# Optimization experiments

Hardware: AMD Instinct MI355X
Metric: run time of the kernel (lower is better)

The kernel has to match this reference:

```python
import jax, jax.numpy as jnp
import numpy as np

N = 8192      # nodes; also input feature dim (x.shape[0] used as in_channels)
E = 524288    # edges per edge type (avg degree 64)
H = 200       # hidden dim (hard-coded in RecomNet)
MEAN_RATING = 3.5


def setup_inputs() -> dict:
    key = jax.random.key(0)
    ks = jax.random.split(key, 14)
    s_in = np.float32(1.0 / np.sqrt(N))
    s_h = np.float32(1.0 / np.sqrt(H))
    return {
        "x": jax.random.normal(ks[0], (N, N), jnp.float32),
        "edge_sim": jax.random.randint(ks[1], (2, E), 0, N),
        "edge_rat": jax.random.randint(ks[2], (2, E), 0, N),
        "mask": jax.random.randint(ks[3], (E,), 0, 2).astype(bool),
        # conv1 params (in=N, out=H)
        "w1_self": jax.random.normal(ks[4], (N, H), jnp.float32) * s_in,
        "w1_sim": jax.random.normal(ks[5], (N, H), jnp.float32) * s_in,
        "w1_rat": jax.random.normal(ks[6], (N, H), jnp.float32) * s_in,
        "b1": jnp.zeros((H,), jnp.float32),
        # conv2 params (in=H, out=H)
        "w2_self": jax.random.normal(ks[7], (H, H), jnp.float32) * s_h,
        "w2_sim": jax.random.normal(ks[8], (H, H), jnp.float32) * s_h,
        "w2_rat": jax.random.normal(ks[9], (H, H), jnp.float32) * s_h,
        "b2": jnp.zeros((H,), jnp.float32),
        # bilinear decoder
        "Q": jax.random.normal(ks[10], (H, H), jnp.float32) * s_h,
    }


def _recom_conv(edge_sim, edge_rat, x, w_self, w_sim, w_rat, b):
    # linear-then-gather-then-scatter (linear commutes with sum aggregation)
    m_sim = (x @ w_sim)[edge_sim[0]]                                   # [E, H]
    agg_sim = jax.ops.segment_sum(m_sim, edge_sim[1], num_segments=N)  # [N, H]
    m_rat = (x @ w_rat)[edge_rat[0]]
    agg_rat = jax.ops.segment_sum(m_rat, edge_rat[1], num_segments=N)
    return x @ w_self + agg_sim + agg_rat + b


def reference(x, w1_self, w1_sim, w1_rat, b1, w2_self, w2_sim, w2_rat, b2, Q,
              edge_sim, edge_rat, mask):
    h = _recom_conv(edge_sim, edge_rat, x, w1_self, w1_sim, w1_rat, b1)
    h = jax.nn.relu(h)
    h = _recom_conv(edge_sim, edge_rat, h, w2_self, w2_sim, w2_rat, b2)
    h1 = h[edge_rat[0]]                                                # [E, H]
    h2 = h[edge_rat[1]]                                                # [E, H]
    pred = jnp.einsum("eh,hk,ek->e", h1, Q, h2) + MEAN_RATING          # [E]
    # original compacts with boolean mask (dynamic shape); here we keep a
    # fixed [E] output and zero out unmasked edges
    return jnp.where(mask, pred, 0.0)
```

## Files before the change

kernel.cpp:

```cpp
#include <hip/hip_runtime.h>

#define NN 8192
#define EE 524288
#define HPAD 256
#define NP 640

using s16x8 = __attribute__((ext_vector_type(8))) short;
using f32x4 = __attribute__((ext_vector_type(4))) float;

__device__ __forceinline__ unsigned short f2b(float f) {
    unsigned u = __float_as_uint(f);
    u = (u + 0x7FFFu + ((u >> 16) & 1u)) >> 16;
    return (unsigned short)u;
}
__device__ __forceinline__ float b2f(unsigned short u) {
    return __uint_as_float((unsigned)u << 16);
}

__device__ __forceinline__ void async16(const unsigned short* g, unsigned short* l)
{
    __builtin_amdgcn_global_load_lds(
        (const __attribute__((address_space(1))) unsigned int*)g,
        (__attribute__((address_space(3))) unsigned int*)l, 16, 0, 0);
}


__global__ void cvt_f2b_kernel(const float* __restrict__ in,
                               unsigned short* __restrict__ out, int n4)
{
    int i = blockIdx.x * 256 + threadIdx.x;
    if (i >= n4) return;
    float4 v = ((const float4*)in)[i];
    ushort4 o;
    o.x = f2b(v.x); o.y = f2b(v.y); o.z = f2b(v.z); o.w = f2b(v.w);
    ((ushort4*)out)[i] = o;
}

__global__ void transpose_w_kernel(const float* __restrict__ w0,
                                   const float* __restrict__ w1,
                                   const float* __restrict__ w2,
                                   unsigned short* __restrict__ out,
                                   int Kout, int Kreal, int Nreal)
{
    __shared__ float tile[32][33];
    const int kb = blockIdx.x << 5;
    const int nb = blockIdx.y << 5;
    const int tx = threadIdx.x, ty = threadIdx.y;
    const int n = nb + tx;
    const float* w = (n < 200) ? w0 : (n < 400) ? w1 : w2;
    const int c = (n < 200) ? n : (n < 400) ? n - 200 : n - 400;
#pragma unroll
    for (int i = 0; i < 4; ++i) {
        const int k = kb + ty + (i << 3);
        float v = 0.f;
        if (n < Nreal && k < Kreal) v = w[(size_t)k * 200 + c];
        tile[ty + (i << 3)][tx] = v;
    }
    __syncthreads();
#pragma unroll
    for (int i = 0; i < 4; ++i) {
        const int nn = nb + ty + (i << 3);
        out[(size_t)nn * Kout + kb + tx] = f2b(tile[tx][ty + (i << 3)]);
    }
}

__global__ __launch_bounds__(256) void gemm_mfma(
    const unsigned short* __restrict__ A,
    const unsigned short* __restrict__ BT,
    float* __restrict__ C, unsigned short* __restrict__ Cb,
    int lda, int KC, int ldc, size_t planeStride,
    float* __restrict__ ys, unsigned short* __restrict__ ysb,
    unsigned short* __restrict__ yrb)
{
    __shared__ unsigned short As[2][128 * 64];
    __shared__ unsigned short Bs[2][128 * 64];
    const int tid  = threadIdx.x;
    const int lane = tid & 63;
    const int w    = tid >> 6;

    const int nx   = gridDim.x;
    const int flat = blockIdx.y * nx + blockIdx.x;
    const int cpx  = (nx * gridDim.y) >> 3;
    const int orig = (flat & 7) * cpx + (flat >> 3);
    const int by   = orig / nx;
    const int bx   = orig - by * nx;

    const int row0 = by << 7;
    const int col0 = bx << 7;
    const int z    = blockIdx.z;
    const int wm = (w >> 1) << 6;
    const int wn = (w & 1) << 6;

    const int sr = lane >> 3;
    const int sc = (lane & 7) ^ sr;
    const size_t kbase = (size_t)z * KC + ((size_t)sc << 3);
    const unsigned short* aG = A  + (size_t)(row0 + w * 8 + sr) * lda + kbase;
    const unsigned short* bG = BT + (size_t)(col0 + w * 8 + sr) * lda + kbase;
    const int ldsOff = w * 8;

    const f32x4 zero = {0.f, 0.f, 0.f, 0.f};
    f32x4 acc[4][4];
#pragma unroll
    for (int i = 0; i < 4; ++i)
#pragma unroll
        for (int j = 0; j < 4; ++j) acc[i][j] = zero;

#pragma unroll
    for (int it = 0; it < 4; ++it) {
        async16(aG + (size_t)(it * 32) * lda, &As[0][(it * 32 + ldsOff) << 6]);
        async16(bG + (size_t)(it * 32) * lda, &Bs[0][(it * 32 + ldsOff) << 6]);
    }
    __syncthreads();

    const int T = KC >> 6;
    for (int t = 0; t < T; ++t) {
        const int cur = t & 1;
        if (t + 1 < T) {
            const int ko = (t + 1) << 6;
#pragma unroll
            for (int it = 0; it < 4; ++it) {
                async16(aG + (size_t)(it * 32) * lda + ko,
                        &As[cur ^ 1][(it * 32 + ldsOff) << 6]);
                async16(bG + (size_t)(it * 32) * lda + ko,
                        &Bs[cur ^ 1][(it * 32 + ldsOff) << 6]);
            }
        }
#pragma unroll
        for (int kk = 0; kk < 2; ++kk) {
            const int q  = (kk << 2) + (lane >> 4);
            const int sl = (q ^ (lane & 7)) << 3;
            s16x8 af[4], bfv[4];
#pragma unroll
            for (int i = 0; i < 4; ++i) {
                const int rm = wm + (i << 4) + (lane & 15);
                af[i]  = *(const s16x8*)(&As[cur][(rm << 6) + sl]);
                const int rn = wn + (i << 4) + (lane & 15);
                bfv[i] = *(const s16x8*)(&Bs[cur][(rn << 6) + sl]);
            }
#pragma unroll
            for (int i = 0; i < 4; ++i)
#pragma unroll
                for (int j = 0; j < 4; ++j)
                    acc[i][j] = __builtin_amdgcn_mfma_f32_16x16x32_bf16(
                        af[i], bfv[j], acc[i][j], 0, 0, 0);
        }
        __syncthreads();
    }

    const int cr = (lane >> 4) << 2;
    const int cc = lane & 15;
    if (ysb) {
#pragma unroll
        for (int i = 0; i < 4; ++i)
#pragma unroll
            for (int j = 0; j < 4; ++j)
#pragma unroll
                for (int r = 0; r < 4; ++r) {
                    const int n = row0 + wm + (i << 4) + cr + r;
                    const int c = col0 + wn + (j << 4) + cc;
                    const float v = acc[i][j][r];
                    if (c < 200)      ys [(size_t)n * 200 + c]        = v;
                    else if (c < 400) ysb[(size_t)n * 200 + (c - 200)] = f2b(v);
                    else if (c < 600) yrb[(size_t)n * 200 + (c - 400)] = f2b(v);
                }
    } else if (Cb) {
#pragma unroll
        for (int i = 0; i < 4; ++i)
#pragma unroll
            for (int j = 0; j < 4; ++j)
#pragma unroll
                for (int r = 0; r < 4; ++r)
                    Cb[(size_t)(row0 + wm + (i << 4) + cr + r) * ldc
                       + (col0 + wn + (j << 4) + cc)] = f2b(acc[i][j][r]);
    } else {
        float* Cp = C + (size_t)z * planeStride;
#pragma unroll
        for (int i = 0; i < 4; ++i)
#pragma unroll
            for (int j = 0; j < 4; ++j)
#pragma unroll
                for (int r = 0; r < 4; ++r)
                    Cp[(size_t)(row0 + wm + (i << 4) + cr + r) * ldc
                       + (col0 + wn + (j << 4) + cc)] = acc[i][j][r];
    }
}

__global__ void combine_kernel(const float* __restrict__ parts, int nplanes,
                               float* __restrict__ y_self,
                               unsigned short* __restrict__ y_simb,
                               unsigned short* __restrict__ y_ratb)
{
    int t = blockIdx.x * 256 + threadIdx.x;
    int n = t / 50, j4 = (t - n * 50) << 2;
    float4 s = {0.f, 0.f, 0.f, 0.f};
    float4 m = {0.f, 0.f, 0.f, 0.f};
    float4 r = {0.f, 0.f, 0.f, 0.f};
    for (int z = 0; z < nplanes; ++z) {
        const float* a = parts + (size_t)z * NN * NP + (size_t)n * NP;
        float4 s2 = *(const float4*)(a + j4);
        float4 m2 = *(const float4*)(a + 200 + j4);
        float4 r2 = *(const float4*)(a + 400 + j4);
        s.x += s2.x; s.y += s2.y; s.z += s2.z; s.w += s2.w;
        m.x += m2.x; m.y += m2.y; m.z += m2.z; m.w += m2.w;
        r.x += r2.x; r.y += r2.y; r.z += r2.z; r.w += r2.w;
    }
    *(float4*)(y_self + (size_t)n * 200 + j4) = s;
    ushort4 mo, ro;
    mo.x = f2b(m.x); mo.y = f2b(m.y); mo.z = f2b(m.z); mo.w = f2b(m.w);
    ro.x = f2b(r.x); ro.y = f2b(r.y); ro.z = f2b(r.z); ro.w = f2b(r.w);
    *(ushort4*)(y_simb + (size_t)n * 200 + j4) = mo;
    *(ushort4*)(y_ratb + (size_t)n * 200 + j4) = ro;
}


__global__ void hist_kernel(const int* __restrict__ e0, const int* __restrict__ e1,
                            int* __restrict__ d0, int* __restrict__ d1)
{
    const int* edges = blockIdx.y ? e1 : e0;
    int* deg = blockIdx.y ? d1 : d0;
    int e = blockIdx.x * 256 + threadIdx.x;
    if (e < EE) atomicAdd(&deg[edges[EE + e]], 1);
}

__global__ void scan_kernel(const int* __restrict__ deg0, int* __restrict__ off0,
                            int* __restrict__ pos0,
                            const int* __restrict__ deg1, int* __restrict__ off1,
                            int* __restrict__ pos1)
{
    const int* deg = blockIdx.x ? deg1 : deg0;
    int* off = blockIdx.x ? off1 : off0;
    int* pos = blockIdx.x ? pos1 : pos0;
    __shared__ int part[256];
    const int t = threadIdx.x;
    const int base = t * 32;
    int s = 0;
#pragma unroll
    for (int i = 0; i < 32; ++i) s += deg[base + i];
    part[t] = s;
    __syncthreads();
    for (int d = 1; d < 256; d <<= 1) {
        int v = (t >= d) ? part[t - d] : 0;
        __syncthreads();
        part[t] += v;
        __syncthreads();
    }
    int run = (t == 0) ? 0 : part[t - 1];
    for (int i = 0; i < 32; ++i) {
        off[base + i] = run;
        pos[base + i] = run;
        run += deg[base + i];
    }
    if (t == 255) off[NN] = run;
}

__global__ void reorder_kernel(const int* __restrict__ e0, int* __restrict__ pos0,
                               int2* __restrict__ se0,
                               const int* __restrict__ e1, int* __restrict__ pos1,
                               int2* __restrict__ se1)
{
    const int* edges = blockIdx.y ? e1 : e0;
    int* pos = blockIdx.y ? pos1 : pos0;
    int2* se = blockIdx.y ? se1 : se0;
    int e = blockIdx.x * 256 + threadIdx.x;
    if (e >= EE) return;
    int p = atomicAdd(&pos[edges[EE + e]], 1);
    se[p] = make_int2(edges[e], e);
}


__device__ __forceinline__ void edge_accum(
    const unsigned short* __restrict__ msg,
    const int* __restrict__ off, const int2* __restrict__ se,
    int n, int w, int j4, bool act, float4& acc)
{
    const int e1 = off[n + 1];
    int i = off[n] + w;
    for (; i + 12 < e1; i += 16) {
        const int s0 = se[i].x;
        const int s1 = se[i + 4].x;
        const int s2 = se[i + 8].x;
        const int s3 = se[i + 12].x;
        if (act) {
            ushort4 v0 = *(const ushort4*)(msg + (size_t)s0 * 200 + j4);
            ushort4 v1 = *(const ushort4*)(msg + (size_t)s1 * 200 + j4);
            ushort4 v2 = *(const ushort4*)(msg + (size_t)s2 * 200 + j4);
            ushort4 v3 = *(const ushort4*)(msg + (size_t)s3 * 200 + j4);
            acc.x += (b2f(v0.x) + b2f(v1.x)) + (b2f(v2.x) + b2f(v3.x));
            acc.y += (b2f(v0.y) + b2f(v1.y)) + (b2f(v2.y) + b2f(v3.y));
            acc.z += (b2f(v0.z) + b2f(v1.z)) + (b2f(v2.z) + b2f(v3.z));
            acc.w += (b2f(v0.w) + b2f(v1.w)) + (b2f(v2.w) + b2f(v3.w));
        }
    }
    for (; i < e1; i += 4) {
        const int s = se[i].x;
        if (act) {
            ushort4 v = *(const ushort4*)(msg + (size_t)s * 200 + j4);
            acc.x += b2f(v.x); acc.y += b2f(v.y);
            acc.z += b2f(v.z); acc.w += b2f(v.w);
        }
    }
}

__global__ __launch_bounds__(256) void agg_fused_kernel(
    const unsigned short* __restrict__ msg_sim,
    const unsigned short* __restrict__ msg_rat,
    const int* __restrict__ off_sim, const int2* __restrict__ se_sim,
    const int* __restrict__ off_rat, const int2* __restrict__ se_rat,
    const float* __restrict__ y_self, const float* __restrict__ bias,
    unsigned short* __restrict__ hb, int relu)
{
    __shared__ float part[4][200];
    const int n = blockIdx.x;
    const int w = threadIdx.x >> 6;
    const int lane = threadIdx.x & 63;
    const int j4 = lane << 2;
    const bool act = lane < 50;

    float4 acc = {0.f, 0.f, 0.f, 0.f};
    edge_accum(msg_sim, off_sim, se_sim, n, w, j4, act, acc);
    edge_accum(msg_rat, off_rat, se_rat, n, w, j4, act, acc);

    if (act) *(float4*)&part[w][j4] = acc;
    __syncthreads();
    const int j = threadIdx.x;
    if (j < 200) {
        float v = part[0][j] + part[1][j] + part[2][j] + part[3][j]
                + y_self[(size_t)n * 200 + j] + bias[j];
        if (relu) v = fmaxf(v, 0.f);
        hb[((size_t)n << 8) + j] = f2b(v);
    } else if (j < HPAD) {
        hb[((size_t)n << 8) + j] = 0;
    }
}

__global__ __launch_bounds__(256) void pred_kernel(
    const unsigned short* __restrict__ hQb,
    const unsigned short* __restrict__ h2b,
    const int* __restrict__ off, const int2* __restrict__ se,
    const int* __restrict__ mask, float* __restrict__ out)
{
    const int n = blockIdx.x;
    const int w = threadIdx.x >> 6;
    const int lane = threadIdx.x & 63;
    float4 b = {0.f, 0.f, 0.f, 0.f};
    if (lane < 50) {
        ushort4 v = *(const ushort4*)(h2b + ((size_t)n << 8) + (lane << 2));
        b.x = b2f(v.x); b.y = b2f(v.y); b.z = b2f(v.z); b.w = b2f(v.w);
    }
    const int e1 = off[n + 1];
    int i = off[n] + w;
    for (; i + 12 < e1; i += 16) {
        const int2 p0 = se[i];
        const int2 p1 = se[i + 4];
        const int2 p2 = se[i + 8];
        const int2 p3 = se[i + 12];
        float s0 = 0.f, s1 = 0.f, s2 = 0.f, s3 = 0.f;
        if (lane < 50) {
            ushort4 a0 = *(const ushort4*)(hQb + ((size_t)p0.x << 8) + (lane << 2));
            ushort4 a1 = *(const ushort4*)(hQb + ((size_t)p1.x << 8) + (lane << 2));
            ushort4 a2 = *(const ushort4*)(hQb + ((size_t)p2.x << 8) + (lane << 2));
            ushort4 a3 = *(const ushort4*)(hQb + ((size_t)p3.x << 8) + (lane << 2));
            s0 = fmaf(b2f(a0.x), b.x, fmaf(b2f(a0.y), b.y,
                 fmaf(b2f(a0.z), b.z, b2f(a0.w) * b.w)));
            s1 = fmaf(b2f(a1.x), b.x, fmaf(b2f(a1.y), b.y,
                 fmaf(b2f(a1.z), b.z, b2f(a1.w) * b.w)));
            s2 = fmaf(b2f(a2.x), b.x, fmaf(b2f(a2.y), b.y,
                 fmaf(b2f(a2.z), b.z, b2f(a2.w) * b.w)));
            s3 = fmaf(b2f(a3.x), b.x, fmaf(b2f(a3.y), b.y,
                 fmaf(b2f(a3.z), b.z, b2f(a3.w) * b.w)));
        }
#pragma unroll
        for (int o = 32; o > 0; o >>= 1) {
            s0 += __shfl_down(s0, o, 64);
            s1 += __shfl_down(s1, o, 64);
            s2 += __shfl_down(s2, o, 64);
            s3 += __shfl_down(s3, o, 64);
        }
        if (lane == 0) {
            out[p0.y] = mask[p0.y] ? (s0 + 3.5f) : 0.f;
            out[p1.y] = mask[p1.y] ? (s1 + 3.5f) : 0.f;
            out[p2.y] = mask[p2.y] ? (s2 + 3.5f) : 0.f;
            out[p3.y] = mask[p3.y] ? (s3 + 3.5f) : 0.f;
        }
    }
    for (; i < e1; i += 4) {
        const int2 p = se[i];
        float s = 0.f;
        if (lane < 50) {
            ushort4 a = *(const ushort4*)(hQb + ((size_t)p.x << 8) + (lane << 2));
            s = fmaf(b2f(a.x), b.x, fmaf(b2f(a.y), b.y,
                fmaf(b2f(a.z), b.z, b2f(a.w) * b.w)));
        }
#pragma unroll
        for (int o = 32; o > 0; o >>= 1) s += __shfl_down(s, o, 64);
        if (lane == 0) out[p.y] = mask[p.y] ? (s + 3.5f) : 0.f;
    }
}

extern "C" void kernel_launch(void* const* d_in, const int* in_sizes, int n_in,
                              void* d_out, int out_size, void* d_ws, size_t ws_size,
                              hipStream_t stream)
{
    const float* x       = (const float*)d_in[0];
    const int*   e_sim   = (const int*)d_in[1];
    const int*   e_rat   = (const int*)d_in[2];
    const int*   mask    = (const int*)d_in[3];
    const float* w1_self = (const float*)d_in[4];
    const float* w1_sim  = (const float*)d_in[5];
    const float* w1_rat  = (const float*)d_in[6];
    const float* b1      = (const float*)d_in[7];
    const float* w2_self = (const float*)d_in[8];
    const float* w2_sim  = (const float*)d_in[9];
    const float* w2_rat  = (const float*)d_in[10];
    const float* b2      = (const float*)d_in[11];
    const float* Q       = (const float*)d_in[12];
    float* out = (float*)d_out;

    char* p = (char*)d_ws;
    auto alloc = [&](size_t bytes) -> char* {
        char* r = p;
        p += (bytes + 255) & ~(size_t)255;
        return r;
    };
    unsigned short* xb    = (unsigned short*)alloc((size_t)NN * NN * 2);
    unsigned short* wbT1  = (unsigned short*)alloc((size_t)NP * NN * 2);
    unsigned short* wbT2  = (unsigned short*)alloc((size_t)NP * HPAD * 2);
    unsigned short* QT    = (unsigned short*)alloc((size_t)HPAD * HPAD * 2);
    float* ypart = (float*)alloc((size_t)4 * NN * NP * 4);
    float* y_self = (float*)alloc((size_t)NN * 200 * 4);
    unsigned short* y_simb = (unsigned short*)alloc((size_t)NN * 200 * 2);
    unsigned short* y_ratb = (unsigned short*)alloc((size_t)NN * 200 * 2);
    unsigned short* h1b = (unsigned short*)alloc((size_t)NN * HPAD * 2);
    unsigned short* h2b = (unsigned short*)alloc((size_t)NN * HPAD * 2);
    unsigned short* hQb = (unsigned short*)alloc((size_t)NN * HPAD * 2);
    int* deg_sim = (int*)alloc(NN * 4);
    int* deg_rat = (int*)alloc(NN * 4);
    int* off_sim = (int*)alloc((NN + 1) * 4);
    int* off_rat = (int*)alloc((NN + 1) * 4);
    int* pos_sim = (int*)alloc(NN * 4);
    int* pos_rat = (int*)alloc(NN * 4);
    int2* se_sim = (int2*)alloc((size_t)EE * 8);
    int2* se_rat = (int2*)alloc((size_t)EE * 8);

    const dim3 blk(256);
    const dim3 tblk(32, 8);

    cvt_f2b_kernel<<<(NN * NN / 4) / 256, blk, 0, stream>>>(x, xb, NN * NN / 4);
    transpose_w_kernel<<<dim3(NN / 32, NP / 32), tblk, 0, stream>>>(
        w1_self, w1_sim, w1_rat, wbT1, NN, NN, 600);
    transpose_w_kernel<<<dim3(HPAD / 32, NP / 32), tblk, 0, stream>>>(
        w2_self, w2_sim, w2_rat, wbT2, HPAD, 200, 600);
    transpose_w_kernel<<<dim3(HPAD / 32, HPAD / 32), tblk, 0, stream>>>(
        Q, Q, Q, QT, HPAD, 200, 200);

    hipMemsetAsync(deg_sim, 0, 2 * NN * 4, stream);
    hist_kernel<<<dim3(EE / 256, 2), blk, 0, stream>>>(e_sim, e_rat, deg_sim, deg_rat);
    scan_kernel<<<2, blk, 0, stream>>>(deg_sim, off_sim, pos_sim,
                                       deg_rat, off_rat, pos_rat);
    reorder_kernel<<<dim3(EE / 256, 2), blk, 0, stream>>>(
        e_sim, pos_sim, se_sim, e_rat, pos_rat, se_rat);

    gemm_mfma<<<dim3(NP / 128, NN / 128, 4), blk, 0, stream>>>(
        xb, wbT1, ypart, nullptr, NN, NN / 4, NP, (size_t)NN * NP,
        nullptr, nullptr, nullptr);
    combine_kernel<<<NN * 50 / 256, blk, 0, stream>>>(
        ypart, 4, y_self, y_simb, y_ratb);
    agg_fused_kernel<<<NN, blk, 0, stream>>>(
        y_simb, y_ratb, off_sim, se_sim, off_rat, se_rat, y_self, b1, h1b, 1);

    gemm_mfma<<<dim3(NP / 128, NN / 128, 1), blk, 0, stream>>>(
        h1b, wbT2, nullptr, nullptr, HPAD, HPAD, NP, 0,
        y_self, y_simb, y_ratb);
    agg_fused_kernel<<<NN, blk, 0, stream>>>(
        y_simb, y_ratb, off_sim, se_sim, off_rat, se_rat, y_self, b2, h2b, 0);

    gemm_mfma<<<dim3(HPAD / 128, NN / 128, 1), blk, 0, stream>>>(
        h2b, QT, nullptr, hQb, HPAD, HPAD, HPAD, 0,
        nullptr, nullptr, nullptr);
    pred_kernel<<<NN, blk, 0, stream>>>(hQb, h2b, off_rat, se_rat, mask, out);
}
```

Baseline: 836.3 us.

## Shrink split-K partials to bf16, merge weight transposes, widen conversion

The split-K partial outputs of the first GEMM are now stored compactly: the self part as fp32 with 200 columns, and the sim/rat parts as bf16 with 400 columns, instead of full 640-wide fp32 planes. The combine kernel reads and sums these smaller planes. The three weight-transpose launches become one 3D-grid launch, and the x fp32-to-bf16 conversion processes 8 elements per thread. The goal is to cut partial-buffer traffic and launch overhead. The cost is extra rounding, since the sim/rat partials are rounded to bf16 before they are summed.

```diff
diff --git a/kernel.cpp b/kernel.cpp
--- a/kernel.cpp
+++ b/kernel.cpp
@@ -4,8 +4,11 @@
 #define EE 524288
 #define HPAD 256
 #define NP 640
+#define PSS ((size_t)NN * 200)
+#define PSM ((size_t)NN * 400)
 
 using s16x8 = __attribute__((ext_vector_type(8))) short;
+using u16x8 = __attribute__((ext_vector_type(8))) unsigned short;
 using f32x4 = __attribute__((ext_vector_type(4))) float;
 
 __device__ __forceinline__ unsigned short f2b(float f) {
@@ -26,25 +29,38 @@
 
 
 __global__ void cvt_f2b_kernel(const float* __restrict__ in,
-                               unsigned short* __restrict__ out, int n4)
+                               unsigned short* __restrict__ out, int n8)
 {
     int i = blockIdx.x * 256 + threadIdx.x;
-    if (i >= n4) return;
-    float4 v = ((const float4*)in)[i];
-    ushort4 o;
-    o.x = f2b(v.x); o.y = f2b(v.y); o.z = f2b(v.z); o.w = f2b(v.w);
-    ((ushort4*)out)[i] = o;
-}
-
-__global__ void transpose_w_kernel(const float* __restrict__ w0,
-                                   const float* __restrict__ w1,
-                                   const float* __restrict__ w2,
-                                   unsigned short* __restrict__ out,
-                                   int Kout, int Kreal, int Nreal)
-{
-    __shared__ float tile[32][33];
+    if (i >= n8) return;
+    float4 v0 = ((const float4*)in)[2 * i];
+    float4 v1 = ((const float4*)in)[2 * i + 1];
+    u16x8 o;
+    o[0] = f2b(v0.x); o[1] = f2b(v0.y); o[2] = f2b(v0.z); o[3] = f2b(v0.w);
+    o[4] = f2b(v1.x); o[5] = f2b(v1.y); o[6] = f2b(v1.z); o[7] = f2b(v1.w);
+    ((u16x8*)out)[i] = o;
+}
+
+__global__ void transpose_w_kernel(
+    const float* __restrict__ u0, const float* __restrict__ u1,
+    const float* __restrict__ u2,
+    const float* __restrict__ v0, const float* __restrict__ v1,
+    const float* __restrict__ v2,
+    const float* __restrict__ Q,
+    unsigned short* __restrict__ o0, unsigned short* __restrict__ o1,
+    unsigned short* __restrict__ o2)
+{
+    const int zc = blockIdx.z;
+    const float *w0, *w1, *w2;
+    unsigned short* out;
+    int Kout, Kreal, Nreal;
+    if (zc == 0)      { w0 = u0; w1 = u1; w2 = u2; out = o0; Kout = NN;   Kreal = NN;  Nreal = 600; }
+    else if (zc == 1) { w0 = v0; w1 = v1; w2 = v2; out = o1; Kout = HPAD; Kreal = 200; Nreal = 600; }
+    else              { w0 = Q;  w1 = Q;  w2 = Q;  out = o2; Kout = HPAD; Kreal = 200; Nreal = 200; }
     const int kb = blockIdx.x << 5;
     const int nb = blockIdx.y << 5;
+    if (kb >= Kout) return;
+    __shared__ float tile[32][33];
     const int tx = threadIdx.x, ty = threadIdx.y;
     const int n = nb + tx;
     const float* w = (n < 200) ? w0 : (n < 400) ? w1 : w2;
@@ -67,10 +83,11 @@
 __global__ __launch_bounds__(256) void gemm_mfma(
     const unsigned short* __restrict__ A,
     const unsigned short* __restrict__ BT,
-    float* __restrict__ C, unsigned short* __restrict__ Cb,
-    int lda, int KC, int ldc, size_t planeStride,
+    int lda, int KC,
+    unsigned short* __restrict__ Cb, int ldc,
     float* __restrict__ ys, unsigned short* __restrict__ ysb,
-    unsigned short* __restrict__ yrb)
+    unsigned short* __restrict__ yrb,
+    float* __restrict__ ysp, unsigned short* __restrict__ ymp)
 {
     __shared__ unsigned short As[2][128 * 64];
     __shared__ unsigned short Bs[2][128 * 64];
@@ -149,7 +166,22 @@
 
     const int cr = (lane >> 4) << 2;
     const int cc = lane & 15;
-    if (ysb) {
+    if (ymp) {
+        float* sp = ysp + (size_t)z * PSS;
+        unsigned short* mp = ymp + (size_t)z * PSM;
+#pragma unroll
+        for (int i = 0; i < 4; ++i)
+#pragma unroll
+            for (int j = 0; j < 4; ++j)
+#pragma unroll
+                for (int r = 0; r < 4; ++r) {
+                    const int n = row0 + wm + (i << 4) + cr + r;
+                    const int c = col0 + wn + (j << 4) + cc;
+                    const float v = acc[i][j][r];
+                    if (c < 200)      sp[(size_t)n * 200 + c] = v;
+                    else if (c < 600) mp[(size_t)n * 400 + (c - 200)] = f2b(v);
+                }
+    } else if (ysb) {
 #pragma unroll
         for (int i = 0; i < 4; ++i)
 #pragma unroll
@@ -163,7 +195,7 @@
                     else if (c < 400) ysb[(size_t)n * 200 + (c - 200)] = f2b(v);
                     else if (c < 600) yrb[(size_t)n * 200 + (c - 400)] = f2b(v);
                 }
-    } else if (Cb) {
+    } else {
 #pragma unroll
         for (int i = 0; i < 4; ++i)
 #pragma unroll
@@ -172,20 +204,11 @@
                 for (int r = 0; r < 4; ++r)
                     Cb[(size_t)(row0 + wm + (i << 4) + cr + r) * ldc
                        + (col0 + wn + (j << 4) + cc)] = f2b(acc[i][j][r]);
-    } else {
-        float* Cp = C + (size_t)z * planeStride;
-#pragma unroll
-        for (int i = 0; i < 4; ++i)
-#pragma unroll
-            for (int j = 0; j < 4; ++j)
-#pragma unroll
-                for (int r = 0; r < 4; ++r)
-                    Cp[(size_t)(row0 + wm + (i << 4) + cr + r) * ldc
-                       + (col0 + wn + (j << 4) + cc)] = acc[i][j][r];
-    }
-}
-
-__global__ void combine_kernel(const float* __restrict__ parts, int nplanes,
+    }
+}
+
+__global__ void combine_kernel(const float* __restrict__ ysp,
+                               const unsigned short* __restrict__ ymp,
                                float* __restrict__ y_self,
                                unsigned short* __restrict__ y_simb,
                                unsigned short* __restrict__ y_ratb)
@@ -195,14 +218,14 @@
     float4 s = {0.f, 0.f, 0.f, 0.f};
     float4 m = {0.f, 0.f, 0.f, 0.f};
     float4 r = {0.f, 0.f, 0.f, 0.f};
-    for (int z = 0; z < nplanes; ++z) {
-        const float* a = parts + (size_t)z * NN * NP + (size_t)n * NP;
-        float4 s2 = *(const float4*)(a + j4);
-        float4 m2 = *(const float4*)(a + 200 + j4);
-        float4 r2 = *(const float4*)(a + 400 + j4);
+#pragma unroll
+    for (int z = 0; z < 4; ++z) {
+        float4 s2 = *(const float4*)(ysp + z * PSS + (size_t)n * 200 + j4);
+        ushort4 m2 = *(const ushort4*)(ymp + z * PSM + (size_t)n * 400 + j4);
+        ushort4 r2 = *(const ushort4*)(ymp + z * PSM + (size_t)n * 400 + 200 + j4);
         s.x += s2.x; s.y += s2.y; s.z += s2.z; s.w += s2.w;
-        m.x += m2.x; m.y += m2.y; m.z += m2.z; m.w += m2.w;
-        r.x += r2.x; r.y += r2.y; r.z += r2.z; r.w += r2.w;
+        m.x += b2f(m2.x); m.y += b2f(m2.y); m.z += b2f(m2.z); m.w += b2f(m2.w);
+        r.x += b2f(r2.x); r.y += b2f(r2.y); r.z += b2f(r2.z); r.w += b2f(r2.w);
     }
     *(float4*)(y_self + (size_t)n * 200 + j4) = s;
     ushort4 mo, ro;
@@ -426,7 +449,8 @@
     unsigned short* wbT1  = (unsigned short*)alloc((size_t)NP * NN * 2);
     unsigned short* wbT2  = (unsigned short*)alloc((size_t)NP * HPAD * 2);
     unsigned short* QT    = (unsigned short*)alloc((size_t)HPAD * HPAD * 2);
-    float* ypart = (float*)alloc((size_t)4 * NN * NP * 4);
+    float* ypart_s = (float*)alloc(4 * PSS * 4);
+    unsigned short* ypart_m = (unsigned short*)alloc(4 * PSM * 2);
     float* y_self = (float*)alloc((size_t)NN * 200 * 4);
     unsigned short* y_simb = (unsigned short*)alloc((size_t)NN * 200 * 2);
     unsigned short* y_ratb = (unsigned short*)alloc((size_t)NN * 200 * 2);
@@ -445,13 +469,9 @@
     const dim3 blk(256);
     const dim3 tblk(32, 8);
 
-    cvt_f2b_kernel<<<(NN * NN / 4) / 256, blk, 0, stream>>>(x, xb, NN * NN / 4);
-    transpose_w_kernel<<<dim3(NN / 32, NP / 32), tblk, 0, stream>>>(
-        w1_self, w1_sim, w1_rat, wbT1, NN, NN, 600);
-    transpose_w_kernel<<<dim3(HPAD / 32, NP / 32), tblk, 0, stream>>>(
-        w2_self, w2_sim, w2_rat, wbT2, HPAD, 200, 600);
-    transpose_w_kernel<<<dim3(HPAD / 32, HPAD / 32), tblk, 0, stream>>>(
-        Q, Q, Q, QT, HPAD, 200, 200);
+    cvt_f2b_kernel<<<(NN * NN / 8) / 256, blk, 0, stream>>>(x, xb, NN * NN / 8);
+    transpose_w_kernel<<<dim3(NN / 32, NP / 32, 3), tblk, 0, stream>>>(
+        w1_self, w1_sim, w1_rat, w2_self, w2_sim, w2_rat, Q, wbT1, wbT2, QT);
 
     hipMemsetAsync(deg_sim, 0, 2 * NN * 4, stream);
     hist_kernel<<<dim3(EE / 256, 2), blk, 0, stream>>>(e_sim, e_rat, deg_sim, deg_rat);
@@ -461,21 +481,21 @@
         e_sim, pos_sim, se_sim, e_rat, pos_rat, se_rat);
 
     gemm_mfma<<<dim3(NP / 128, NN / 128, 4), blk, 0, stream>>>(
-        xb, wbT1, ypart, nullptr, NN, NN / 4, NP, (size_t)NN * NP,
-        nullptr, nullptr, nullptr);
+        xb, wbT1, NN, NN / 4, nullptr, 0,
+        nullptr, nullptr, nullptr, ypart_s, ypart_m);
     combine_kernel<<<NN * 50 / 256, blk, 0, stream>>>(
-        ypart, 4, y_self, y_simb, y_ratb);
+        ypart_s, ypart_m, y_self, y_simb, y_ratb);
     agg_fused_kernel<<<NN, blk, 0, stream>>>(
         y_simb, y_ratb, off_sim, se_sim, off_rat, se_rat, y_self, b1, h1b, 1);
 
     gemm_mfma<<<dim3(NP / 128, NN / 128, 1), blk, 0, stream>>>(
-        h1b, wbT2, nullptr, nullptr, HPAD, HPAD, NP, 0,
-        y_self, y_simb, y_ratb);
+        h1b, wbT2, HPAD, HPAD, nullptr, 0,
+        y_self, y_simb, y_ratb, nullptr, nullptr);
     agg_fused_kernel<<<NN, blk, 0, stream>>>(
         y_simb, y_ratb, off_sim, se_sim, off_rat, se_rat, y_self, b2, h2b, 0);
 
     gemm_mfma<<<dim3(HPAD / 128, NN / 128, 1), blk, 0, stream>>>(
-        h2b, QT, nullptr, hQb, HPAD, HPAD, HPAD, 0,
-        nullptr, nullptr, nullptr);
+        h2b, QT, HPAD, HPAD, hQb, HPAD,
+        nullptr, nullptr, nullptr, nullptr, nullptr);
     pred_kernel<<<NN, blk, 0, stream>>>(hQb, h2b, off_rat, se_rat, mask, out);
 }
```

Result: no change. 833.6 us (-0.3%).
